# Performance work log

Measured on AMD Instinct MI355X. Metric: run time of the kernel, lower is better.

The kernel has to match this reference:

```python
import jax, jax.numpy as jnp
import numpy as np

BANK_FILTERS = 64
DIM = 128
KSIZE = 3
BATCH = 256


def setup_inputs() -> dict:
    key = jax.random.key(0)
    k1, k2 = jax.random.split(key)
    bank_request = jax.random.normal(k1, (BATCH, BANK_FILTERS), dtype=jnp.float32)
    weight = jax.random.normal(k2, (BANK_FILTERS, DIM, DIM, KSIZE, KSIZE), dtype=jnp.float32)
    return {"bank_request": bank_request, "weight": weight}


def reference(bank_request, weight):
    # softmax over filter bank, then weighted sum of filters -> per-sample kernel
    probs = jax.nn.softmax(bank_request, axis=1)          # (B, F)
    Fb, D1, D2, K1, K2 = weight.shape
    # express as a single GEMM over the filter axis instead of broadcast-mul-reduce
    w2d = weight.reshape(Fb, D1 * D2 * K1 * K2)           # (F, D*D*k*k)
    kernel = probs @ w2d                                   # (B, D*D*k*k)
    return kernel.reshape(bank_request.shape[0], D1, D2, K1, K2)
```

## Files before the change

kernel.cpp:

```cpp
#include <hip/hip_runtime.h>
#include <math.h>

#define BATCH 256
#define FB    64
#define NCOL  147456
#define TPB   256
#define BT    32

typedef float vfloat4 __attribute__((ext_vector_type(4)));

__global__ void softmax_t(const float* __restrict__ x, float* __restrict__ pt) {
    const int b = blockIdx.x;
    const int lane = threadIdx.x;
    float v = x[b * FB + lane];
    float m = v;
#pragma unroll
    for (int o = 32; o > 0; o >>= 1) m = fmaxf(m, __shfl_xor(m, o));
    float e = __expf(v - m);
    float s = e;
#pragma unroll
    for (int o = 32; o > 0; o >>= 1) s += __shfl_xor(s, o);
    pt[lane * BATCH + b] = e / s;
}

__global__ __launch_bounds__(TPB, 2) void bank_gemm(
        const float* __restrict__ W, const float* __restrict__ PT,
        float* __restrict__ out) {
    const int tid = threadIdx.x;
    const int ncol4 = NCOL / 4;
    const vfloat4* __restrict__ Wv = (const vfloat4*)W;
    const int c4 = blockIdx.x * TPB + tid;
    const int bg = blockIdx.y;
    const float* __restrict__ P0 = PT + bg * BT;

    vfloat4 acc[BT];
#pragma unroll
    for (int b = 0; b < BT; ++b) acc[b] = (vfloat4)(0.f);

    vfloat4 w = Wv[c4];
    for (int f = 0; f < FB; ++f) {
        vfloat4 wn = w;
        if (f + 1 < FB) wn = Wv[(f + 1) * ncol4 + c4];
        const float* __restrict__ pr = P0 + f * BATCH;
#pragma unroll
        for (int b = 0; b < BT; ++b) {
            const float p = pr[b];
            acc[b] = w * p + acc[b];
        }
        w = wn;
    }

    vfloat4* Ov = (vfloat4*)out;
    const long long obase = (long long)(bg * BT) * ncol4 + c4;
#pragma unroll
    for (int b = 0; b < BT; ++b) {
        __builtin_nontemporal_store(acc[b], &Ov[obase + (long long)b * ncol4]);
    }
}

extern "C" void kernel_launch(void* const* d_in, const int* in_sizes, int n_in,
                              void* d_out, int out_size, void* d_ws, size_t ws_size,
                              hipStream_t stream) {
    const float* bank   = (const float*)d_in[0];
    const float* weight = (const float*)d_in[1];
    float* out    = (float*)d_out;
    float* probsT = (float*)d_ws;

    softmax_t<<<BATCH, FB, 0, stream>>>(bank, probsT);

    dim3 grid(NCOL / (TPB * 4), BATCH / BT);
    bank_gemm<<<grid, TPB, 0, stream>>>(weight, probsT, out);
}
```

Measured before the change: 222.0 us.

## Use bf16 MFMA for bank GEMM with LDS-staged weight tiles

Replaces the fp32 FMA outer-product GEMM with bf16 MFMA 16x16x32 instructions. Softmax probabilities and weights are rounded to bf16, and each block stages a 64-column weight slice in padded LDS. Each column block now loops over the whole batch, so weights are read once instead of once per batch group. The output write (about 151 MB of fp32) still dominates, and the stores become scalar, which may hurt write coalescing. bf16 rounding also lowers accuracy.

```diff
diff --git a/kernel.cpp b/kernel.cpp
--- a/kernel.cpp
+++ b/kernel.cpp
@@ -5,11 +5,19 @@
 #define FB    64
 #define NCOL  147456
 #define TPB   256
-#define BT    32
+#define NB    64
+#define PAD   72
 
-typedef float vfloat4 __attribute__((ext_vector_type(4)));
+typedef short short8 __attribute__((ext_vector_type(8)));
+typedef float f32x4  __attribute__((ext_vector_type(4)));
 
-__global__ void softmax_t(const float* __restrict__ x, float* __restrict__ pt) {
+static __device__ __forceinline__ unsigned short f2bf(float x) {
+    unsigned int u = __float_as_uint(x);
+    unsigned int r = (u + 0x7FFF + ((u >> 16) & 1)) >> 16;
+    return (unsigned short)r;
+}
+
+__global__ void softmax_bf16(const float* __restrict__ x, unsigned short* __restrict__ p) {
     const int b = blockIdx.x;
     const int lane = threadIdx.x;
     float v = x[b * FB + lane];
@@ -20,41 +28,57 @@
     float s = e;
 #pragma unroll
     for (int o = 32; o > 0; o >>= 1) s += __shfl_xor(s, o);
-    pt[lane * BATCH + b] = e / s;
+    p[b * FB + lane] = f2bf(e / s);
 }
 
-__global__ __launch_bounds__(TPB, 2) void bank_gemm(
-        const float* __restrict__ W, const float* __restrict__ PT,
+__global__ __launch_bounds__(TPB) void bank_gemm_mfma(
+        const float* __restrict__ W, const unsigned short* __restrict__ P,
         float* __restrict__ out) {
+    __shared__ __align__(16) unsigned short Wt[NB * PAD];
+
     const int tid = threadIdx.x;
-    const int ncol4 = NCOL / 4;
-    const vfloat4* __restrict__ Wv = (const vfloat4*)W;
-    const int c4 = blockIdx.x * TPB + tid;
-    const int bg = blockIdx.y;
-    const float* __restrict__ P0 = PT + bg * BT;
+    const int n0  = blockIdx.x * NB;
 
-    vfloat4 acc[BT];
+    const float* __restrict__ Wp = W + n0;
 #pragma unroll
-    for (int b = 0; b < BT; ++b) acc[b] = (vfloat4)(0.f);
+    for (int i = 0; i < 8; ++i) {
+        const int e2 = i * 256 + tid;
+        const int f2 = e2 >> 6;
+        const int n  = e2 & 63;
+        const float a = Wp[(2 * f2)     * NCOL + n];
+        const float b = Wp[(2 * f2 + 1) * NCOL + n];
+        const unsigned int pk = (unsigned int)f2bf(a) | ((unsigned int)f2bf(b) << 16);
+        *(unsigned int*)&Wt[n * PAD + 2 * f2] = pk;
+    }
+    __syncthreads();
 
-    vfloat4 w = Wv[c4];
-    for (int f = 0; f < FB; ++f) {
-        vfloat4 wn = w;
-        if (f + 1 < FB) wn = Wv[(f + 1) * ncol4 + c4];
-        const float* __restrict__ pr = P0 + f * BATCH;
+    const int l  = tid & 63;
+    const int w  = tid >> 6;
+    const int nq = l & 15;
+    const int q  = l >> 4;
+    const int nw = w * 16 + nq;
+
+    const short8 b0 = *(const short8*)&Wt[nw * PAD + q * 8];
+    const short8 b1 = *(const short8*)&Wt[nw * PAD + 32 + q * 8];
+
+    const int ncol_n = n0 + nw;
+    float* __restrict__ ob = out + ncol_n;
+
+#pragma unroll 4
+    for (int bt = 0; bt < BATCH / 16; ++bt) {
+        const int off = (bt * 16 + nq) * FB + q * 8;
+        const short8 a0 = *(const short8*)(P + off);
+        const short8 a1 = *(const short8*)(P + off + 32);
+
+        f32x4 d = {0.f, 0.f, 0.f, 0.f};
+        d = __builtin_amdgcn_mfma_f32_16x16x32_bf16(a0, b0, d, 0, 0, 0);
+        d = __builtin_amdgcn_mfma_f32_16x16x32_bf16(a1, b1, d, 0, 0, 0);
+
+        const int bb = bt * 16 + q * 4;
 #pragma unroll
-        for (int b = 0; b < BT; ++b) {
-            const float p = pr[b];
-            acc[b] = w * p + acc[b];
+        for (int r = 0; r < 4; ++r) {
+            __builtin_nontemporal_store(d[r], ob + (long long)(bb + r) * NCOL);
         }
-        w = wn;
-    }
-
-    vfloat4* Ov = (vfloat4*)out;
-    const long long obase = (long long)(bg * BT) * ncol4 + c4;
-#pragma unroll
-    for (int b = 0; b < BT; ++b) {
-        __builtin_nontemporal_store(acc[b], &Ov[obase + (long long)b * ncol4]);
     }
 }
 
@@ -63,11 +87,9 @@
                               hipStream_t stream) {
     const float* bank   = (const float*)d_in[0];
     const float* weight = (const float*)d_in[1];
-    float* out    = (float*)d_out;
-    float* probsT = (float*)d_ws;
+    float* out = (float*)d_out;
+    unsigned short* probs = (unsigned short*)d_ws;
 
-    softmax_t<<<BATCH, FB, 0, stream>>>(bank, probsT);
-
-    dim3 grid(NCOL / (TPB * 4), BATCH / BT);
-    bank_gemm<<<grid, TPB, 0, stream>>>(weight, probsT, out);
+    softmax_bf16<<<BATCH, FB, 0, stream>>>(bank, probs);
+    bank_gemm_mfma<<<NCOL / NB, TPB, 0, stream>>>(weight, probs, out);
 }
```

Result: no change. 223.6 us (+0.7%).
